# Kernel optimization log

Measured on AMD Instinct MI355X. Metric: run time of the kernel, lower is better.

The kernel has to match this reference:

```python
import jax, jax.numpy as jnp
import numpy as np

S, B, C = 7, 2, 4
N = 5 * B + C
LAMBDA_BOX = LAMBDA_CLS = LAMBDA_DF = 1.0
BATCH = 16384


def setup_inputs() -> dict:
    key = jax.random.key(0)
    k1, k2, k3 = jax.random.split(key, 3)
    shape = (BATCH, S, S, N)
    pred = jax.random.uniform(k1, shape, jnp.float32, 0.02, 0.98)
    target = jax.random.uniform(k2, shape, jnp.float32, 0.02, 0.98)
    obj = (jax.random.uniform(k3, (BATCH, S, S)) < 0.3).astype(jnp.float32)
    # confidence channels of both target bboxes carry the 0/1 object indicator
    target = target.at[..., 4].set(obj).at[..., 9].set(obj)
    return {"pred_tensor": pred, "target_tensor": target}


def _bce(p, t):
    # elementwise binary cross entropy (sum applied by caller)
    return -(t * jnp.log(p) + (1.0 - t) * jnp.log(1.0 - p))


def reference(pred_tensor, target_tensor):
    conf_t = target_tensor[..., 4]                       # [b,S,S]
    coord = (conf_t > 0).astype(pred_tensor.dtype)       # object cells

    pb = pred_tensor[..., :5 * B].reshape(*pred_tensor.shape[:-1], B, 5)   # [b,S,S,B,5]
    tb = target_tensor[..., :5 * B].reshape(*target_tensor.shape[:-1], B, 5)

    # xywh (cell coords) -> xyxy (image coords), as in the torch loop
    p_xy = pb[..., :2] / S
    p_wh = pb[..., 2:4]
    p_lt = p_xy - 0.5 * p_wh
    p_rb = p_xy + 0.5 * p_wh
    t0 = tb[..., 0, :]                                   # first target box of the group
    t_xy = t0[..., :2] / S
    t_wh = t0[..., 2:4]
    t_lt = t_xy - 0.5 * t_wh
    t_rb = t_xy + 0.5 * t_wh

    lt = jnp.maximum(p_lt, t_lt[..., None, :])
    rb = jnp.minimum(p_rb, t_rb[..., None, :])
    wh = jnp.clip(rb - lt, 0.0)
    inter = wh[..., 0] * wh[..., 1]                      # [b,S,S,B]
    area_p = (p_rb[..., 0] - p_lt[..., 0]) * (p_rb[..., 1] - p_lt[..., 1])
    area_t = ((t_rb[..., 0] - t_lt[..., 0]) * (t_rb[..., 1] - t_lt[..., 1]))[..., None]
    iou = inter / (area_p + area_t - inter)              # [b,S,S,B]

    max_iou = jnp.max(iou, axis=-1)                      # [b,S,S]
    idx = jnp.argmax(iou, axis=-1)                       # responsible bbox index
    resp_p = jnp.take_along_axis(pb, idx[..., None, None], axis=-2)[..., 0, :]  # [b,S,S,5]
    resp_t = jnp.take_along_axis(tb, idx[..., None, None], axis=-2)[..., 0, :]

    loss_xy = jnp.sum(coord * jnp.sum((resp_p[..., :2] - resp_t[..., :2]) ** 2, -1))
    loss_wh = jnp.sum(coord * jnp.sum((jnp.sqrt(resp_p[..., 2:4]) - jnp.sqrt(resp_t[..., 2:4])) ** 2, -1))
    loss_obj = jnp.sum(coord * (resp_p[..., 4] - max_iou) ** 2)

    loss_cls = jnp.sum(coord[..., None] * _bce(pred_tensor[..., 5 * B:], target_tensor[..., 5 * B:]))

    # focal-style df term over ALL cells (the original triple loop)
    q = conf_t
    p = pred_tensor[..., 4]
    alpha = (1.0 - q) / (1.0 - p)
    loss_df = jnp.sum(alpha * (p - q) * jnp.log(p) + (q - p) * jnp.log(1.0 - p))

    total = LAMBDA_BOX * (loss_xy + loss_wh + loss_obj) + LAMBDA_CLS * loss_cls + LAMBDA_DF * loss_df
    return total
```

## Files before the change

### kernel.cpp

```cpp
#include <hip/hip_runtime.h>


#define NCELLS (16384 * 7 * 7)
#define NPAIRS (NCELLS / 2)
#define TPB 256

__device__ __forceinline__ float cell_loss(const float* __restrict__ p,
                                           const float* __restrict__ t) {
    const float conf_t = t[4];
    const float coord = (conf_t > 0.0f) ? 1.0f : 0.0f;

    const float tx = t[0] / 7.0f;
    const float ty = t[1] / 7.0f;
    const float tw = t[2];
    const float th = t[3];
    const float tlx = tx - 0.5f * tw, tly = ty - 0.5f * th;
    const float trx = tx + 0.5f * tw, trY = ty + 0.5f * th;
    const float area_t = (trx - tlx) * (trY - tly);

    float iou0, iou1;
    {
        const float px = p[0] / 7.0f, py = p[1] / 7.0f;
        const float pw = p[2], ph = p[3];
        const float plx = px - 0.5f * pw, ply = py - 0.5f * ph;
        const float prx = px + 0.5f * pw, prY = py + 0.5f * ph;
        const float ltx = fmaxf(plx, tlx), lty = fmaxf(ply, tly);
        const float rbx = fminf(prx, trx), rby = fminf(prY, trY);
        const float wx = fmaxf(rbx - ltx, 0.0f), wy = fmaxf(rby - lty, 0.0f);
        const float inter = wx * wy;
        const float area_p = (prx - plx) * (prY - ply);
        iou0 = inter / (area_p + area_t - inter);
    }
    {
        const float px = p[5] / 7.0f, py = p[6] / 7.0f;
        const float pw = p[7], ph = p[8];
        const float plx = px - 0.5f * pw, ply = py - 0.5f * ph;
        const float prx = px + 0.5f * pw, prY = py + 0.5f * ph;
        const float ltx = fmaxf(plx, tlx), lty = fmaxf(ply, tly);
        const float rbx = fminf(prx, trx), rby = fminf(prY, trY);
        const float wx = fmaxf(rbx - ltx, 0.0f), wy = fmaxf(rby - lty, 0.0f);
        const float inter = wx * wy;
        const float area_p = (prx - plx) * (prY - ply);
        iou1 = inter / (area_p + area_t - inter);
    }

    const bool sel1 = (iou1 > iou0);
    const float max_iou = fmaxf(iou0, iou1);

    const float rp0 = sel1 ? p[5] : p[0];
    const float rp1 = sel1 ? p[6] : p[1];
    const float rp2 = sel1 ? p[7] : p[2];
    const float rp3 = sel1 ? p[8] : p[3];
    const float rp4 = sel1 ? p[9] : p[4];
    const float rt0 = sel1 ? t[5] : t[0];
    const float rt1 = sel1 ? t[6] : t[1];
    const float rt2 = sel1 ? t[7] : t[2];
    const float rt3 = sel1 ? t[8] : t[3];

    const float dx = rp0 - rt0;
    const float dy = rp1 - rt1;
    const float l_xy = dx * dx + dy * dy;

    const float sw = sqrtf(rp2) - sqrtf(rt2);
    const float sh = sqrtf(rp3) - sqrtf(rt3);
    const float l_wh = sw * sw + sh * sh;

    const float dobj = rp4 - max_iou;
    const float l_obj = dobj * dobj;

    float l_cls = 0.0f;
#pragma unroll
    for (int c = 10; c < 14; ++c) {
        const float pc = p[c];
        const float tc = t[c];
        l_cls += -(tc * logf(pc) + (1.0f - tc) * logf(1.0f - pc));
    }

    const float q = conf_t;
    const float pp = p[4];
    const float alpha = (1.0f - q) / (1.0f - pp);
    const float l_df = alpha * (pp - q) * logf(pp) + (q - pp) * logf(1.0f - pp);

    return coord * (l_xy + l_wh + l_obj + l_cls) + l_df;
}

__global__ __launch_bounds__(TPB) void yolo_loss_kernel(
    const float* __restrict__ pred, const float* __restrict__ tgt,
    float* __restrict__ out) {
    const int pair = blockIdx.x * TPB + threadIdx.x;

    float lp[28];
    float lt[28];
    {
        const float4* __restrict__ p4 =
            reinterpret_cast<const float4*>(pred) + (long)pair * 7;
        const float4* __restrict__ t4 =
            reinterpret_cast<const float4*>(tgt) + (long)pair * 7;
#pragma unroll
        for (int i = 0; i < 7; ++i) {
            reinterpret_cast<float4*>(lp)[i] = p4[i];
            reinterpret_cast<float4*>(lt)[i] = t4[i];
        }
    }

    float v = cell_loss(lp, lt) + cell_loss(lp + 14, lt + 14);

#pragma unroll
    for (int off = 32; off > 0; off >>= 1) v += __shfl_down(v, off, 64);

    __shared__ float wsum[TPB / 64];
    const int lane = threadIdx.x & 63;
    const int wid = threadIdx.x >> 6;
    if (lane == 0) wsum[wid] = v;
    __syncthreads();
    if (threadIdx.x == 0) {
        float s = wsum[0] + wsum[1] + wsum[2] + wsum[3];
        atomicAdd(out, s);
    }
}

extern "C" void kernel_launch(void* const* d_in, const int* in_sizes, int n_in,
                              void* d_out, int out_size, void* d_ws, size_t ws_size,
                              hipStream_t stream) {
    const float* pred = (const float*)d_in[0];
    const float* tgt  = (const float*)d_in[1];
    float* out = (float*)d_out;

    hipMemsetAsync(out, 0, sizeof(float), stream);

    const int blocks = NPAIRS / TPB;
    yolo_loss_kernel<<<blocks, TPB, 0, stream>>>(pred, tgt, out);
}
```

Baseline: 119.0 us.

## Stage inputs through LDS with coalesced direct global-to-LDS loads

Replaces the strided per-thread float4 loads, where each thread read 7 consecutive float4s at a 112-byte stride, with wave-coalesced global_load_lds transfers into shared memory. Each thread then reads its own 7 float4s back from LDS. The aim is better global memory coalescing. In exchange it adds about 57 KB of LDS per block, which limits occupancy, plus a block barrier, and the strided LDS reads may cause bank conflicts.

```diff
diff --git a/kernel.cpp b/kernel.cpp
--- a/kernel.cpp
+++ b/kernel.cpp
@@ -4,6 +4,11 @@
 #define NCELLS (16384 * 7 * 7)
 #define NPAIRS (NCELLS / 2)
 #define TPB 256
+#define PPB 256
+#define SLOTS (PPB * 7)
+
+typedef __attribute__((address_space(3))) void lds_void;
+typedef const __attribute__((address_space(1))) void glb_void;
 
 __device__ __forceinline__ float cell_loss(const float* __restrict__ p,
                                            const float* __restrict__ t) {
@@ -87,20 +92,34 @@
 __global__ __launch_bounds__(TPB) void yolo_loss_kernel(
     const float* __restrict__ pred, const float* __restrict__ tgt,
     float* __restrict__ out) {
-    const int pair = blockIdx.x * TPB + threadIdx.x;
+    __shared__ float4 sp[SLOTS];
+    __shared__ float4 st[SLOTS];
+
+    const int tid = threadIdx.x;
+    const int wid = tid >> 6;
+    const int lane = tid & 63;
+
+    const long base4 = (long)blockIdx.x * SLOTS;
+    const float4* __restrict__ gp = reinterpret_cast<const float4*>(pred) + base4;
+    const float4* __restrict__ gt = reinterpret_cast<const float4*>(tgt) + base4;
+
+#pragma unroll
+    for (int it = 0; it < 7; ++it) {
+        const int s = wid * 448 + it * 64;
+        __builtin_amdgcn_global_load_lds((glb_void*)(gp + s + lane),
+                                         (lds_void*)(sp + s), 16, 0, 0);
+        __builtin_amdgcn_global_load_lds((glb_void*)(gt + s + lane),
+                                         (lds_void*)(st + s), 16, 0, 0);
+    }
+    __syncthreads();
 
     float lp[28];
     float lt[28];
-    {
-        const float4* __restrict__ p4 =
-            reinterpret_cast<const float4*>(pred) + (long)pair * 7;
-        const float4* __restrict__ t4 =
-            reinterpret_cast<const float4*>(tgt) + (long)pair * 7;
 #pragma unroll
-        for (int i = 0; i < 7; ++i) {
-            reinterpret_cast<float4*>(lp)[i] = p4[i];
-            reinterpret_cast<float4*>(lt)[i] = t4[i];
-        }
+    for (int j = 0; j < 7; ++j) {
+        const int s = 7 * tid + j;
+        reinterpret_cast<float4*>(lp)[j] = sp[s];
+        reinterpret_cast<float4*>(lt)[j] = st[s];
     }
 
     float v = cell_loss(lp, lt) + cell_loss(lp + 14, lt + 14);
@@ -109,11 +128,9 @@
     for (int off = 32; off > 0; off >>= 1) v += __shfl_down(v, off, 64);
 
     __shared__ float wsum[TPB / 64];
-    const int lane = threadIdx.x & 63;
-    const int wid = threadIdx.x >> 6;
     if (lane == 0) wsum[wid] = v;
     __syncthreads();
-    if (threadIdx.x == 0) {
+    if (tid == 0) {
         float s = wsum[0] + wsum[1] + wsum[2] + wsum[3];
         atomicAdd(out, s);
     }
```

New measurement: 117.1 us. About the same (-1.5%).
